# Kernel tuning notes

Hardware: AMD Instinct MI355X
Metric: run time of the kernel (lower is better)

## Reference

```python
import jax, jax.numpy as jnp
import numpy as np

B, N, C, M, OUT = 4, 256, 32, 4, 64


def _uniform(k, shape, fan_in):
    s = 1.0 / np.sqrt(fan_in)
    return jax.random.uniform(k, shape, jnp.float32, -s, s)


def setup_inputs() -> dict:
    key = jax.random.key(0)
    ks = jax.random.split(key, 11)
    return {
        "x": jax.random.normal(ks[0], (B, N, N, C), jnp.float32),
        # Neighborhood / SnConv2to1 linears (in=C, out=M neighborhood channels)
        "w1_nb": _uniform(ks[1], (3 * C, M), 3 * C),
        "b1_nb": _uniform(ks[2], (M,), 3 * C),
        "w0_nb": _uniform(ks[3], (2 * C, M), 2 * C),
        "b0_nb": _uniform(ks[4], (M,), 2 * C),
        # SnConv2 linears (in channels = M*C after neighborhood product)
        "w2d": _uniform(ks[5], (2 * M * C, OUT), 2 * M * C),
        "b2d": _uniform(ks[6], (OUT,), 2 * M * C),
        "w1d": _uniform(ks[7], (3 * M * C, OUT), 3 * M * C),
        "b1d": _uniform(ks[8], (OUT,), 3 * M * C),
        "w0d": _uniform(ks[9], (2 * M * C, OUT), 2 * M * C),
        "b0d": _uniform(ks[10], (OUT,), 2 * M * C),
    }


def _contractions(x):
    # x: [B, n, n, c]; mask=None, reduction='mean' path of _get_contractions
    n = x.shape[1]
    rowsum = x.sum(axis=1) / n                      # [B, n, c]
    colsum = x.sum(axis=2) / n                      # [B, n, c]
    diag = jnp.diagonal(x, axis1=1, axis2=2)        # [B, c, n]
    rowcolsum = x.sum(axis=(1, 2)) / (n * n)        # [B, c]
    diag_sum = diag.sum(axis=-1) / n                # [B, c]  (/= sqrt(n^2))
    diag = jnp.moveaxis(diag, -1, 1)                # move_from_end -> [B, n, c]
    return rowsum, colsum, diag, rowcolsum, diag_sum


def reference(x, w1_nb, b1_nb, w0_nb, b0_nb, w2d, b2d, w1d, b1d, w0d, b0d):
    # ---- Neighborhood: SnConv2to1 -> sigmoid ----
    rs, cs, dg, rcs, ds = _contractions(x)
    obj1 = jnp.concatenate([rs, cs, dg], axis=-1)             # [B, n, 3C]
    obj0 = jnp.concatenate([rcs, ds], axis=-1)                # [B, 2C]
    node = obj1 @ w1_nb + b1_nb + (obj0 @ w0_nb + b0_nb)[:, None, :]
    neighbs = jax.nn.sigmoid(node)                            # [B, n, M]
    # ---- _neighbor_elementwise_product ----
    expanded = neighbs[:, None, :, :] * neighbs[:, :, None, :]  # [B, n, n, M]
    # channel_product: outer product over channel dims, collapsed to M*C
    xl = (expanded[..., :, None] * x[..., None, :]).reshape(B, N, N, M * C)
    # ---- SnConv2 on the localized tensor ----
    rs2, cs2, dg2, rcs2, ds2 = _contractions(xl)
    obj2d = jnp.concatenate([xl, jnp.swapaxes(xl, 1, 2)], axis=-1)  # [B,n,n,2MC]
    obj1d = jnp.concatenate([rs2, cs2, dg2], axis=-1)               # [B,n,3MC]
    obj0d = jnp.concatenate([rcs2, ds2], axis=-1)                   # [B,2MC]
    out = (obj2d @ w2d + b2d
           + (obj1d @ w1d + b1d)[:, None, :, :]
           + (obj0d @ w0d + b0d)[:, None, None, :])                 # [B,n,n,OUT]
    return out
```

## Files before the change

kernel.cpp:

```cpp
#include <hip/hip_runtime.h>
#include <math.h>

#define Bv 4
#define Nv 256
#define Cv 32
#define Mv 4
#define OUTv 64
#define MCv (Mv*Cv)

typedef _Float16 h8 __attribute__((ext_vector_type(8)));
typedef _Float16 h4 __attribute__((ext_vector_type(4)));
typedef float f4 __attribute__((ext_vector_type(4)));

__device__ __align__(16) float g_xT  [Bv * Nv * Nv * Cv];
__device__ __align__(16) float g_csP [8 * Bv * Nv * Cv];
__device__ __align__(16) float g_rs  [Bv * Nv * Cv];
__device__ __align__(16) float g_cs  [Bv * Nv * Cv];
__device__ __align__(16) float g_dgx [Bv * Nv * Cv];
__device__ __align__(16) float g_nb  [Bv * Nv * Mv];
__device__ __align__(16) float g_rcs2R[8 * Bv * MCv];
__device__ __align__(16) float g_ds2R [8 * Bv * MCv];
__device__ __align__(16) float g_addv[Bv * Nv * OUTv];
__device__ __align__(16) _Float16 g_wfrag[8 * 4 * 64 * 8];

__global__ __launch_bounds__(256) void k_transpose(const float* __restrict__ x) {
    int it = blockIdx.x, jt = blockIdx.y, b = blockIdx.z;
    int i0 = it * 8, j0 = jt * 32;
    int t = threadIdx.x;
    __shared__ __align__(16) float4 T[32 * 65];
    const float4* x4  = (const float4*)(x    + (size_t)b * Nv * Nv * Cv);
    float4*       xT4 = (float4*)      (g_xT + (size_t)b * Nv * Nv * Cv);
    #pragma unroll
    for (int r = 0; r < 8; r++) {
        int j = t >> 3, c4 = t & 7;
        T[j * 65 + r * 8 + c4] = x4[((size_t)(i0 + r) * Nv + j0 + j) * 8 + c4];
    }
    __syncthreads();
    #pragma unroll
    for (int r = 0; r < 8; r++) {
        int idx = r * 256 + t;
        int j = idx >> 6, i = (idx >> 3) & 7, c4 = idx & 7;
        xT4[((size_t)(j0 + j) * Nv + i0 + i) * 8 + c4] = T[j * 65 + i * 8 + c4];
    }
    {
        int r = t >> 5, c = t & 31;
        const float* Tf = (const float*)T;
        float s = 0.f;
        #pragma unroll
        for (int j = 0; j < 32; j++) s += Tf[j * 260 + r * 32 + c];
        g_csP[((size_t)jt * Bv + b) * Nv * Cv + (i0 + r) * Cv + c] = s;
    }
}

__global__ __launch_bounds__(256) void k_contract1(const float* __restrict__ x,
                                                   const float* __restrict__ w2d) {
    int bx = blockIdx.x, b = blockIdx.y;
    int t = threadIdx.x;
    if (bx >= Nv) {
        if (b != 0) return;
        int r = bx - Nv;
        if (r == 8) {
            float4 z = {0.f,0.f,0.f,0.f};
            #pragma unroll
            for (int k = 0; k < 4; k++) {
                ((float4*)g_rcs2R)[k * 256 + t] = z;
                ((float4*)g_ds2R )[k * 256 + t] = z;
            }
            return;
        }
        int fi = r * 256 + t;
        int s = fi >> 8, q = (fi >> 6) & 3, lane = fi & 63;
        int k0 = s * 32 + ((lane >> 4) << 3);
        int o = q * 16 + (lane & 15);
        #pragma unroll
        for (int jj = 0; jj < 8; jj++)
            g_wfrag[fi * 8 + jj] = (_Float16)w2d[(size_t)(k0 + jj) * OUTv + o];
        return;
    }
    int c4 = t & 7, sub = t >> 3;
    __shared__ float red[32][36];
    float4 acc = {0.f,0.f,0.f,0.f};
    int n = bx;
    const float4* xT4 = (const float4*)(g_xT + (size_t)b * Nv * Nv * Cv);
    for (int i = sub; i < Nv; i += 32) {
        float4 v = xT4[((size_t)n * Nv + i) * 8 + c4];
        acc.x += v.x; acc.y += v.y; acc.z += v.z; acc.w += v.w;
    }
    red[sub][c4*4+0] = acc.x; red[sub][c4*4+1] = acc.y;
    red[sub][c4*4+2] = acc.z; red[sub][c4*4+3] = acc.w;
    __syncthreads();
    if (t < 32) {
        float s = 0.f;
        #pragma unroll
        for (int k = 0; k < 32; k++) s += red[k][t];
        g_rs[(b * Nv + n) * Cv + t] = s * (1.0f / Nv);
        float csv = 0.f;
        #pragma unroll
        for (int p = 0; p < 8; p++)
            csv += g_csP[((size_t)p * Bv + b) * Nv * Cv + n * Cv + t];
        g_cs[(b * Nv + n) * Cv + t] = csv * (1.0f / Nv);
    }
    if (t < 8) {
        const float4* xb4 = (const float4*)(x + (size_t)b * Nv * Nv * Cv);
        ((float4*)g_dgx)[(b * Nv + n) * 8 + t] = xb4[((size_t)n * Nv + n) * 8 + t];
    }
}

__global__ void k_neighb(const float* __restrict__ w1, const float* __restrict__ b1,
                         const float* __restrict__ w0, const float* __restrict__ b0) {
    int b = blockIdx.x, t = threadIdx.x;
    int c = t & 31, sub = t >> 5;
    float ar = 0.f, ad = 0.f;
    for (int n = sub; n < Nv; n += 8) {
        ar += g_rs[(b * Nv + n) * Cv + c];
        ad += g_dgx[(b * Nv + n) * Cv + c];
    }
    __shared__ float red[8][64];
    __shared__ float obj0[64];
    __shared__ float redm[64][4];
    __shared__ float t0nb[4];
    red[sub][c] = ar;
    red[sub][32 + c] = ad;
    __syncthreads();
    if (t < 64) {
        float s = 0.f;
        #pragma unroll
        for (int k = 0; k < 8; k++) s += red[k][t];
        obj0[t] = s * (1.0f / Nv);
    }
    __syncthreads();
    {
        int k = t >> 2, m = t & 3;
        redm[k][m] = obj0[k] * w0[k * Mv + m];
    }
    __syncthreads();
    if (t < 4) {
        float v = b0[t];
        #pragma unroll
        for (int k = 0; k < 64; k++) v += redm[k][t];
        t0nb[t] = v;
    }
    __syncthreads();
    int n = t;
    float node[4];
    #pragma unroll
    for (int m = 0; m < 4; m++) node[m] = t0nb[m] + b1[m];
    for (int cc = 0; cc < Cv; cc++) {
        float r = g_rs[(b * Nv + n) * Cv + cc];
        float s = g_cs[(b * Nv + n) * Cv + cc];
        float d = g_dgx[(b * Nv + n) * Cv + cc];
        #pragma unroll
        for (int m = 0; m < 4; m++)
            node[m] += r * w1[cc * Mv + m] + s * w1[(Cv + cc) * Mv + m] + d * w1[(2 * Cv + cc) * Mv + m];
    }
    #pragma unroll
    for (int m = 0; m < 4; m++)
        g_nb[(b * Nv + n) * Mv + m] = 1.0f / (1.0f + expf(-node[m]));
}

__global__ __launch_bounds__(256) void k_fused(const float* __restrict__ x,
    const float* __restrict__ w1d, const float* __restrict__ b1d,
    const float* __restrict__ b2d, const float* __restrict__ b0d) {
    int n = blockIdx.x, b = blockIdx.y;
    int t = threadIdx.x;

    __shared__ __align__(16) float4 nb4[Nv];
    __shared__ float red[2][16][132];
    __shared__ float S1l[MCv], S2l[MCv];
    __shared__ float redD[4][64];

    nb4[t] = ((const float4*)g_nb)[b * Nv + t];
    __syncthreads();

    int half = t >> 7, tt = t & 127, c4 = tt & 7, sub = tt >> 3;
    const float4* src4 = half
        ? (const float4*)(x    + (size_t)b * Nv * Nv * Cv) + (size_t)n * Nv * 8
        : (const float4*)(g_xT + (size_t)b * Nv * Nv * Cv) + (size_t)n * Nv * 8;
    float4 a[4];
    #pragma unroll
    for (int m = 0; m < 4; m++) a[m] = {0.f,0.f,0.f,0.f};
    for (int i = sub; i < Nv; i += 16) {
        float4 v = src4[i * 8 + c4];
        float4 nv = nb4[i];
        a[0].x += nv.x*v.x; a[0].y += nv.x*v.y; a[0].z += nv.x*v.z; a[0].w += nv.x*v.w;
        a[1].x += nv.y*v.x; a[1].y += nv.y*v.y; a[1].z += nv.y*v.z; a[1].w += nv.y*v.w;
        a[2].x += nv.z*v.x; a[2].y += nv.z*v.y; a[2].z += nv.z*v.z; a[2].w += nv.z*v.w;
        a[3].x += nv.w*v.x; a[3].y += nv.w*v.y; a[3].z += nv.w*v.z; a[3].w += nv.w*v.w;
    }
    #pragma unroll
    for (int m = 0; m < 4; m++) {
        red[half][sub][m*32 + c4*4+0] = a[m].x; red[half][sub][m*32 + c4*4+1] = a[m].y;
        red[half][sub][m*32 + c4*4+2] = a[m].z; red[half][sub][m*32 + c4*4+3] = a[m].w;
    }
    __syncthreads();
    if (t < 128) {
        float s = 0.f;
        #pragma unroll
        for (int k = 0; k < 16; k++) s += red[0][k][t];
        S1l[t] = s;
        int m = t >> 5, c = t & 31;
        float nv = ((const float*)&nb4[n])[m];
        int rep = ((n & 7) * Bv + b) * MCv + t;
        atomicAdd(&g_rcs2R[rep], nv * s);
        atomicAdd(&g_ds2R [rep], nv * nv * g_dgx[(b * Nv + n) * Cv + c]);
    } else {
        int u = t - 128;
        float s = 0.f;
        #pragma unroll
        for (int k = 0; k < 16; k++) s += red[1][k][u];
        S2l[u] = s;
    }
    __syncthreads();

    {
        int o = t & 63, ks = t >> 6;
        const float invN = 1.0f / Nv;
        float nv = ((const float*)&nb4[n])[ks];
        float f = nv * invN, d2 = nv * nv;
        const float* dgr = g_dgx + (size_t)(b * Nv + n) * Cv;
        float acc = 0.f;
        #pragma unroll 8
        for (int cc = 0; cc < 32; cc++) {
            int mc = ks * 32 + cc;
            acc += f * S1l[mc] * w1d[(size_t)mc * OUTv + o]
                 + f * S2l[mc] * w1d[(size_t)(MCv + mc) * OUTv + o]
                 + d2 * dgr[cc] * w1d[(size_t)(2 * MCv + mc) * OUTv + o];
        }
        redD[ks][o] = acc;
    }
    __syncthreads();
    if (t < 64) {
        float v = redD[0][t] + redD[1][t] + redD[2][t] + redD[3][t]
                + b1d[t] + b2d[t] + b0d[t];
        g_addv[(size_t)(b * Nv + n) * OUTv + t] = v;
    }
}

#define XPAD 40
__global__ __launch_bounds__(256) void k_main(const float* __restrict__ x,
                                              float* __restrict__ out,
                                              const float* __restrict__ w0d) {
    int jt = blockIdx.x, ip = blockIdx.y, b = blockIdx.z;
    int i0 = ip * 2, i1 = i0 + 1;
    int j0 = jt * 128;
    int t = threadIdx.x;
    int lane = t & 63, w = t >> 6;
    int rowA = lane & 15, quad = lane >> 4;

    __shared__ __align__(16) _Float16 Wl[8 * 4 * 64 * 8];
    __shared__ __align__(16) _Float16 Xt0[128 * XPAD];
    __shared__ __align__(16) _Float16 Xb0[128 * XPAD];
    __shared__ __align__(16) _Float16 Xt1[128 * XPAD];
    __shared__ __align__(16) _Float16 Xb1[128 * XPAD];
    __shared__ float rcl[MCv], dsl[MCv];
    __shared__ float t0red[4][64];
    __shared__ float t0l[64];

    {
        const float4* src = (const float4*)g_wfrag;
        float4* dst = (float4*)Wl;
        #pragma unroll
        for (int r = 0; r < 8; r++) dst[r * 256 + t] = src[r * 256 + t];
    }
    {
        const float4* x4  = (const float4*)x;
        const float4* xT4 = (const float4*)g_xT;
        #pragma unroll
        for (int r = 0; r < 4; r++) {
            int idx = r * 256 + t;
            int j = idx >> 3, c4 = idx & 7;
            float4 v0 = x4 [((size_t)(b * Nv + i0) * Nv + j0 + j) * 8 + c4];
            float4 v1 = x4 [((size_t)(b * Nv + i1) * Nv + j0 + j) * 8 + c4];
            float4 u0 = xT4[((size_t)(b * Nv + i0) * Nv + j0 + j) * 8 + c4];
            float4 u1 = xT4[((size_t)(b * Nv + i1) * Nv + j0 + j) * 8 + c4];
            h4 h0; h0[0] = (_Float16)v0.x; h0[1] = (_Float16)v0.y;
            h0[2] = (_Float16)v0.z; h0[3] = (_Float16)v0.w;
            *(h4*)&Xt0[j * XPAD + c4 * 4] = h0;
            h4 h1; h1[0] = (_Float16)v1.x; h1[1] = (_Float16)v1.y;
            h1[2] = (_Float16)v1.z; h1[3] = (_Float16)v1.w;
            *(h4*)&Xt1[j * XPAD + c4 * 4] = h1;
            h4 g0; g0[0] = (_Float16)u0.x; g0[1] = (_Float16)u0.y;
            g0[2] = (_Float16)u0.z; g0[3] = (_Float16)u0.w;
            *(h4*)&Xb0[j * XPAD + c4 * 4] = g0;
            h4 g1; g1[0] = (_Float16)u1.x; g1[1] = (_Float16)u1.y;
            g1[2] = (_Float16)u1.z; g1[3] = (_Float16)u1.w;
            *(h4*)&Xb1[j * XPAD + c4 * 4] = g1;
        }
    }
    if (t < 128) {
        float s = 0.f;
        #pragma unroll
        for (int r = 0; r < 8; r++) s += g_rcs2R[(r * Bv + b) * MCv + t];
        rcl[t] = s;
    } else {
        int tt = t - 128;
        float s = 0.f;
        #pragma unroll
        for (int r = 0; r < 8; r++) s += g_ds2R[(r * Bv + b) * MCv + tt];
        dsl[tt] = s;
    }
    int jl1 = w * 32 + rowA, jl2 = jl1 + 16;
    _Float16 e1h0[4], e2h0[4], e1h1[4], e2h1[4];
    {
        const float* ni0 = g_nb + (size_t)(b * Nv + i0) * Mv;
        const float* ni1 = g_nb + (size_t)(b * Nv + i1) * Mv;
        const float* n1 = g_nb + (size_t)(b * Nv + j0 + jl1) * Mv;
        const float* n2 = g_nb + (size_t)(b * Nv + j0 + jl2) * Mv;
        #pragma unroll
        for (int m = 0; m < 4; m++) {
            e1h0[m] = (_Float16)(ni0[m] * n1[m]);
            e2h0[m] = (_Float16)(ni0[m] * n2[m]);
            e1h1[m] = (_Float16)(ni1[m] * n1[m]);
            e2h1[m] = (_Float16)(ni1[m] * n2[m]);
        }
    }
    __syncthreads();
    {
        int o = t & 63, ks = t >> 6;
        const float invN = 1.0f / Nv;
        const float invN2 = invN * invN;
        float a0 = 0.f;
        #pragma unroll 8
        for (int cc = 0; cc < 32; cc++) {
            int mc = ks * 32 + cc;
            a0 += invN2 * rcl[mc] * w0d[(size_t)mc * OUTv + o]
                + invN  * dsl[mc] * w0d[(size_t)(MCv + mc) * OUTv + o];
        }
        t0red[ks][o] = a0;
    }
    __syncthreads();
    if (t < 64) t0l[t] = t0red[0][t] + t0red[1][t] + t0red[2][t] + t0red[3][t];
    __syncthreads();

    f4 acc[2][2][4];
    #pragma unroll
    for (int ii = 0; ii < 2; ii++)
        #pragma unroll
        for (int js = 0; js < 2; js++)
            #pragma unroll
            for (int q = 0; q < 4; q++) acc[ii][js][q] = {0.f, 0.f, 0.f, 0.f};

    const h8* Wf = (const h8*)Wl;
    #pragma unroll
    for (int part = 0; part < 2; part++) {
        const _Float16* X0 = part ? Xb0 : Xt0;
        const _Float16* X1 = part ? Xb1 : Xt1;
        h8 xv1_0 = *(const h8*)&X0[jl1 * XPAD + quad * 8];
        h8 xv2_0 = *(const h8*)&X0[jl2 * XPAD + quad * 8];
        h8 xv1_1 = *(const h8*)&X1[jl1 * XPAD + quad * 8];
        h8 xv2_1 = *(const h8*)&X1[jl2 * XPAD + quad * 8];
        #pragma unroll
        for (int m = 0; m < 4; m++) {
            h8 a1_0 = xv1_0 * e1h0[m];
            h8 a2_0 = xv2_0 * e2h0[m];
            h8 a1_1 = xv1_1 * e1h1[m];
            h8 a2_1 = xv2_1 * e2h1[m];
            int s = part * 4 + m;
            #pragma unroll
            for (int q = 0; q < 4; q++) {
                h8 bf = Wf[(s * 4 + q) * 64 + lane];
                acc[0][0][q] = __builtin_amdgcn_mfma_f32_16x16x32_f16(a1_0, bf, acc[0][0][q], 0, 0, 0);
                acc[0][1][q] = __builtin_amdgcn_mfma_f32_16x16x32_f16(a2_0, bf, acc[0][1][q], 0, 0, 0);
                acc[1][0][q] = __builtin_amdgcn_mfma_f32_16x16x32_f16(a1_1, bf, acc[1][0][q], 0, 0, 0);
                acc[1][1][q] = __builtin_amdgcn_mfma_f32_16x16x32_f16(a2_1, bf, acc[1][1][q], 0, 0, 0);
            }
        }
    }
    #pragma unroll
    for (int js = 0; js < 2; js++) {
        int jbase = j0 + w * 32 + js * 16 + quad * 4;
        #pragma unroll
        for (int q = 0; q < 4; q++) {
            int o = q * 16 + rowA;
            float tv = t0l[o];
            #pragma unroll
            for (int r = 0; r < 4; r++) {
                int j = jbase + r;
                float av = g_addv[(size_t)(b * Nv + j) * OUTv + o] + tv;
                out[(((size_t)(b * Nv + i0)) * Nv + j) * OUTv + o] = acc[0][js][q][r] + av;
                out[(((size_t)(b * Nv + i1)) * Nv + j) * OUTv + o] = acc[1][js][q][r] + av;
            }
        }
    }
}

extern "C" void kernel_launch(void* const* d_in, const int* in_sizes, int n_in,
                              void* d_out, int out_size, void* d_ws, size_t ws_size,
                              hipStream_t stream) {
    const float* x     = (const float*)d_in[0];
    const float* w1_nb = (const float*)d_in[1];
    const float* b1_nb = (const float*)d_in[2];
    const float* w0_nb = (const float*)d_in[3];
    const float* b0_nb = (const float*)d_in[4];
    const float* w2d   = (const float*)d_in[5];
    const float* b2d   = (const float*)d_in[6];
    const float* w1d   = (const float*)d_in[7];
    const float* b1d   = (const float*)d_in[8];
    const float* w0d   = (const float*)d_in[9];
    const float* b0d   = (const float*)d_in[10];
    float* out = (float*)d_out;
    (void)d_ws; (void)ws_size;

    hipLaunchKernelGGL(k_transpose, dim3(Nv / 8, Nv / 32, Bv), dim3(256), 0, stream, x);
    hipLaunchKernelGGL(k_contract1, dim3(Nv + 9, Bv), dim3(256), 0, stream, x, w2d);
    hipLaunchKernelGGL(k_neighb, dim3(Bv), dim3(256), 0, stream,
                       w1_nb, b1_nb, w0_nb, b0_nb);
    hipLaunchKernelGGL(k_fused, dim3(Nv, Bv), dim3(256), 0, stream,
                       x, w1d, b1d, b2d, b0d);
    hipLaunchKernelGGL(k_main, dim3(2, Nv / 2, Bv), dim3(256), 0, stream, x, out, w0d);
}
```

Before: 177.2 us.

## Drop explicit transpose kernel and read x with strided access instead

Removes the k_transpose kernel and its 32 MB transposed copy g_xT, along with the partial column-sum buffer. Row and column sums become separate block ranges in k_contract1 that read x directly. k_fused and k_main now fetch transposed elements from x with strided 128-byte chunks. This saves one full write and re-read of the input plus one launch, at the cost of less contiguous access in the consumers.

```diff
diff --git a/kernel.cpp b/kernel.cpp
--- a/kernel.cpp
+++ b/kernel.cpp
@@ -12,8 +12,6 @@
 typedef _Float16 h4 __attribute__((ext_vector_type(4)));
 typedef float f4 __attribute__((ext_vector_type(4)));
 
-__device__ __align__(16) float g_xT  [Bv * Nv * Nv * Cv];
-__device__ __align__(16) float g_csP [8 * Bv * Nv * Cv];
 __device__ __align__(16) float g_rs  [Bv * Nv * Cv];
 __device__ __align__(16) float g_cs  [Bv * Nv * Cv];
 __device__ __align__(16) float g_dgx [Bv * Nv * Cv];
@@ -23,42 +21,13 @@
 __device__ __align__(16) float g_addv[Bv * Nv * OUTv];
 __device__ __align__(16) _Float16 g_wfrag[8 * 4 * 64 * 8];
 
-__global__ __launch_bounds__(256) void k_transpose(const float* __restrict__ x) {
-    int it = blockIdx.x, jt = blockIdx.y, b = blockIdx.z;
-    int i0 = it * 8, j0 = jt * 32;
-    int t = threadIdx.x;
-    __shared__ __align__(16) float4 T[32 * 65];
-    const float4* x4  = (const float4*)(x    + (size_t)b * Nv * Nv * Cv);
-    float4*       xT4 = (float4*)      (g_xT + (size_t)b * Nv * Nv * Cv);
-    #pragma unroll
-    for (int r = 0; r < 8; r++) {
-        int j = t >> 3, c4 = t & 7;
-        T[j * 65 + r * 8 + c4] = x4[((size_t)(i0 + r) * Nv + j0 + j) * 8 + c4];
-    }
-    __syncthreads();
-    #pragma unroll
-    for (int r = 0; r < 8; r++) {
-        int idx = r * 256 + t;
-        int j = idx >> 6, i = (idx >> 3) & 7, c4 = idx & 7;
-        xT4[((size_t)(j0 + j) * Nv + i0 + i) * 8 + c4] = T[j * 65 + i * 8 + c4];
-    }
-    {
-        int r = t >> 5, c = t & 31;
-        const float* Tf = (const float*)T;
-        float s = 0.f;
-        #pragma unroll
-        for (int j = 0; j < 32; j++) s += Tf[j * 260 + r * 32 + c];
-        g_csP[((size_t)jt * Bv + b) * Nv * Cv + (i0 + r) * Cv + c] = s;
-    }
-}
-
 __global__ __launch_bounds__(256) void k_contract1(const float* __restrict__ x,
                                                    const float* __restrict__ w2d) {
     int bx = blockIdx.x, b = blockIdx.y;
     int t = threadIdx.x;
-    if (bx >= Nv) {
+    if (bx >= 2 * Nv) {
         if (b != 0) return;
-        int r = bx - Nv;
+        int r = bx - 2 * Nv;
         if (r == 8) {
             float4 z = {0.f,0.f,0.f,0.f};
             #pragma unroll
@@ -78,31 +47,40 @@
         return;
     }
     int c4 = t & 7, sub = t >> 3;
+    const float4* xb4 = (const float4*)(x + (size_t)b * Nv * Nv * Cv);
     __shared__ float red[32][36];
     float4 acc = {0.f,0.f,0.f,0.f};
-    int n = bx;
-    const float4* xT4 = (const float4*)(g_xT + (size_t)b * Nv * Nv * Cv);
-    for (int i = sub; i < Nv; i += 32) {
-        float4 v = xT4[((size_t)n * Nv + i) * 8 + c4];
-        acc.x += v.x; acc.y += v.y; acc.z += v.z; acc.w += v.w;
-    }
-    red[sub][c4*4+0] = acc.x; red[sub][c4*4+1] = acc.y;
-    red[sub][c4*4+2] = acc.z; red[sub][c4*4+3] = acc.w;
-    __syncthreads();
-    if (t < 32) {
-        float s = 0.f;
-        #pragma unroll
-        for (int k = 0; k < 32; k++) s += red[k][t];
-        g_rs[(b * Nv + n) * Cv + t] = s * (1.0f / Nv);
-        float csv = 0.f;
-        #pragma unroll
-        for (int p = 0; p < 8; p++)
-            csv += g_csP[((size_t)p * Bv + b) * Nv * Cv + n * Cv + t];
-        g_cs[(b * Nv + n) * Cv + t] = csv * (1.0f / Nv);
-    }
-    if (t < 8) {
-        const float4* xb4 = (const float4*)(x + (size_t)b * Nv * Nv * Cv);
-        ((float4*)g_dgx)[(b * Nv + n) * 8 + t] = xb4[((size_t)n * Nv + n) * 8 + t];
+    if (bx < Nv) {
+        int n = bx;
+        for (int i = sub; i < Nv; i += 32) {
+            float4 v = xb4[((size_t)i * Nv + n) * 8 + c4];
+            acc.x += v.x; acc.y += v.y; acc.z += v.z; acc.w += v.w;
+        }
+        red[sub][c4*4+0] = acc.x; red[sub][c4*4+1] = acc.y;
+        red[sub][c4*4+2] = acc.z; red[sub][c4*4+3] = acc.w;
+        __syncthreads();
+        if (t < 32) {
+            float s = 0.f;
+            #pragma unroll
+            for (int k = 0; k < 32; k++) s += red[k][t];
+            g_rs[(b * Nv + n) * Cv + t] = s * (1.0f / Nv);
+        }
+        if (t < 8) ((float4*)g_dgx)[(b * Nv + n) * 8 + t] = xb4[((size_t)n * Nv + n) * 8 + t];
+    } else {
+        int n = bx - Nv;
+        for (int j = sub; j < Nv; j += 32) {
+            float4 v = xb4[((size_t)n * Nv + j) * 8 + c4];
+            acc.x += v.x; acc.y += v.y; acc.z += v.z; acc.w += v.w;
+        }
+        red[sub][c4*4+0] = acc.x; red[sub][c4*4+1] = acc.y;
+        red[sub][c4*4+2] = acc.z; red[sub][c4*4+3] = acc.w;
+        __syncthreads();
+        if (t < 32) {
+            float s = 0.f;
+            #pragma unroll
+            for (int k = 0; k < 32; k++) s += red[k][t];
+            g_cs[(b * Nv + n) * Cv + t] = s * (1.0f / Nv);
+        }
     }
 }
 
@@ -172,15 +150,14 @@
     nb4[t] = ((const float4*)g_nb)[b * Nv + t];
     __syncthreads();
 
+    const float4* xb4 = (const float4*)(x + (size_t)b * Nv * Nv * Cv);
     int half = t >> 7, tt = t & 127, c4 = tt & 7, sub = tt >> 3;
-    const float4* src4 = half
-        ? (const float4*)(x    + (size_t)b * Nv * Nv * Cv) + (size_t)n * Nv * 8
-        : (const float4*)(g_xT + (size_t)b * Nv * Nv * Cv) + (size_t)n * Nv * 8;
     float4 a[4];
     #pragma unroll
     for (int m = 0; m < 4; m++) a[m] = {0.f,0.f,0.f,0.f};
     for (int i = sub; i < Nv; i += 16) {
-        float4 v = src4[i * 8 + c4];
+        float4 v = half ? xb4[((size_t)n * Nv + i) * 8 + c4]
+                        : xb4[((size_t)i * Nv + n) * 8 + c4];
         float4 nv = nb4[i];
         a[0].x += nv.x*v.x; a[0].y += nv.x*v.y; a[0].z += nv.x*v.z; a[0].w += nv.x*v.w;
         a[1].x += nv.y*v.x; a[1].y += nv.y*v.y; a[1].z += nv.y*v.z; a[1].w += nv.y*v.w;
@@ -263,16 +240,15 @@
         for (int r = 0; r < 8; r++) dst[r * 256 + t] = src[r * 256 + t];
     }
     {
-        const float4* x4  = (const float4*)x;
-        const float4* xT4 = (const float4*)g_xT;
+        const float4* x4 = (const float4*)x;
         #pragma unroll
         for (int r = 0; r < 4; r++) {
             int idx = r * 256 + t;
             int j = idx >> 3, c4 = idx & 7;
-            float4 v0 = x4 [((size_t)(b * Nv + i0) * Nv + j0 + j) * 8 + c4];
-            float4 v1 = x4 [((size_t)(b * Nv + i1) * Nv + j0 + j) * 8 + c4];
-            float4 u0 = xT4[((size_t)(b * Nv + i0) * Nv + j0 + j) * 8 + c4];
-            float4 u1 = xT4[((size_t)(b * Nv + i1) * Nv + j0 + j) * 8 + c4];
+            float4 v0 = x4[((size_t)(b * Nv + i0) * Nv + j0 + j) * 8 + c4];
+            float4 v1 = x4[((size_t)(b * Nv + i1) * Nv + j0 + j) * 8 + c4];
+            float4 u0 = x4[((size_t)(b * Nv + j0 + j) * Nv + i0) * 8 + c4];
+            float4 u1 = x4[((size_t)(b * Nv + j0 + j) * Nv + i1) * 8 + c4];
             h4 h0; h0[0] = (_Float16)v0.x; h0[1] = (_Float16)v0.y;
             h0[2] = (_Float16)v0.z; h0[3] = (_Float16)v0.w;
             *(h4*)&Xt0[j * XPAD + c4 * 4] = h0;
@@ -401,8 +377,7 @@
     float* out = (float*)d_out;
     (void)d_ws; (void)ws_size;
 
-    hipLaunchKernelGGL(k_transpose, dim3(Nv / 8, Nv / 32, Bv), dim3(256), 0, stream, x);
-    hipLaunchKernelGGL(k_contract1, dim3(Nv + 9, Bv), dim3(256), 0, stream, x, w2d);
+    hipLaunchKernelGGL(k_contract1, dim3(2 * Nv + 9, Bv), dim3(256), 0, stream, x, w2d);
     hipLaunchKernelGGL(k_neighb, dim3(Bv), dim3(256), 0, stream,
                        w1_nb, b1_nb, w0_nb, b0_nb);
     hipLaunchKernelGGL(k_fused, dim3(Nv, Bv), dim3(256), 0, stream,
```

Result: faster. 167.3 us (-5.6%).
